# Optimization experiments

Measured on AMD Instinct MI355X. Metric: run time of the kernel, lower is better.

## Reference

```python
import jax, jax.numpy as jnp
import numpy as np

B, S, Z, C, V = 4, 8192, 1024, 1024, 8192
HC, HS, L, NB = 1, 8, 2, 2  # cross heads, self heads, self-attends per block, blocks


def setup_inputs() -> dict:
    key = jax.random.key(0)
    ks = iter(jax.random.split(key, 80))
    nrm = lambda shape, s=0.02: jax.random.normal(next(ks), shape, jnp.float32) * s
    inp = {}
    inp['inputs'] = jax.random.randint(next(ks), (B, S), 0, V)
    inp['emb'] = nrm((V, C))
    inp['c_lnq_g'] = jnp.ones((C,)); inp['c_lnq_b'] = jnp.zeros((C,))
    inp['c_lnkv_g'] = jnp.ones((C,)); inp['c_lnkv_b'] = jnp.zeros((C,))
    for n in ['q', 'k', 'v', 'o']:
        inp[f'c_w{n}'] = nrm((C, C)); inp[f'c_b{n}'] = jnp.zeros((C,))
    inp['c_ln2_g'] = jnp.ones((C,)); inp['c_ln2_b'] = jnp.zeros((C,))
    inp['c_w1'] = nrm((C, C)); inp['c_b1'] = jnp.zeros((C,))
    inp['c_w2'] = nrm((C, C)); inp['c_b2'] = jnp.zeros((C,))
    inp['s_lnq_g'] = jnp.ones((L, C)); inp['s_lnq_b'] = jnp.zeros((L, C))
    for n in ['q', 'k', 'v', 'o']:
        inp[f's_w{n}'] = nrm((L, C, C)); inp[f's_b{n}'] = jnp.zeros((L, C))
    inp['s_ln2_g'] = jnp.ones((L, C)); inp['s_ln2_b'] = jnp.zeros((L, C))
    inp['s_w1'] = nrm((L, C, C)); inp['s_b1'] = jnp.zeros((L, C))
    inp['s_w2'] = nrm((L, C, C)); inp['s_b2'] = jnp.zeros((L, C))
    return inp


def _ln(x, g, b):
    m = x.mean(-1, keepdims=True)
    v = ((x - m) ** 2).mean(-1, keepdims=True)
    return (x - m) * jax.lax.rsqrt(v + 1e-5) * g + b


def _sqrelu(x):
    r = jax.nn.relu(x)
    return r * r


def _attn(qx, kvx, wq, bq, wk, bk, wv, bv, wo, bo, h, mask):
    b, lq, c = qx.shape
    lk = kvx.shape[1]
    d = c // h
    q = (qx @ wq + bq).reshape(b, lq, h, d)
    k = (kvx @ wk + bk).reshape(b, lk, h, d)
    v = (kvx @ wv + bv).reshape(b, lk, h, d)
    s = jnp.einsum('bqhd,bkhd->bhqk', q, k) * (1.0 / np.sqrt(d))
    s = jnp.where(mask, s, jnp.finfo(s.dtype).min)
    a = jax.nn.softmax(s, axis=-1)
    o = jnp.einsum('bhqk,bkhd->bqhd', a, v).reshape(b, lq, c)
    return o @ wo + bo


def _forward(inputs, emb,
             c_lnq_g, c_lnq_b, c_lnkv_g, c_lnkv_b,
             c_wq, c_bq, c_wk, c_bk, c_wv, c_bv, c_wo, c_bo,
             c_ln2_g, c_ln2_b, c_w1, c_b1, c_w2, c_b2,
             s_lnq_g, s_lnq_b, s_wq, s_bq, s_wk, s_bk, s_wv, s_bv, s_wo, s_bo,
             s_ln2_g, s_ln2_b, s_w1, s_b1, s_w2, s_b2):
    e = emb[inputs]                     # [B, S, C] embedded long context
    z = e[:, -Z:, :]                    # latents = last Z embedded positions
    # Perceiver-AR shifted causal cross mask: latent i sits at abs pos (S - Z + i)
    qi = jnp.arange(Z)[:, None]
    ki = jnp.arange(S)[None, :]
    cmask = ki <= (S - Z) + qi          # True = attend allowed, [Z, S]
    zn = _ln(z, c_lnq_g, c_lnq_b)
    en = _ln(e, c_lnkv_g, c_lnkv_b)
    z = z + _attn(zn, en, c_wq, c_bq, c_wk, c_bk, c_wv, c_bv, c_wo, c_bo, HC, cmask)
    h = _ln(z, c_ln2_g, c_ln2_b)
    z = z + _sqrelu(h @ c_w1 + c_b1) @ c_w2 + c_b2
    smask = jnp.tril(jnp.ones((Z, Z), bool))
    for _ in range(NB):                 # weight-shared blocks
        for l in range(L):
            zn = _ln(z, s_lnq_g[l], s_lnq_b[l])
            z = z + _attn(zn, zn, s_wq[l], s_bq[l], s_wk[l], s_bk[l],
                          s_wv[l], s_bv[l], s_wo[l], s_bo[l], HS, smask)
            h = _ln(z, s_ln2_g[l], s_ln2_b[l])
            z = z + _sqrelu(h @ s_w1[l] + s_b1[l]) @ s_w2[l] + s_b2[l]
    return z


def reference(inputs, emb,
              c_lnq_g, c_lnq_b, c_lnkv_g, c_lnkv_b,
              c_wq, c_bq, c_wk, c_bk, c_wv, c_bv, c_wo, c_bo,
              c_ln2_g, c_ln2_b, c_w1, c_b1, c_w2, c_b2,
              s_lnq_g, s_lnq_b, s_wq, s_bq, s_wk, s_bk, s_wv, s_bv, s_wo, s_bo,
              s_ln2_g, s_ln2_b, s_w1, s_b1, s_w2, s_b2):
    return _forward(inputs, emb,
                    c_lnq_g, c_lnq_b, c_lnkv_g, c_lnkv_b,
                    c_wq, c_bq, c_wk, c_bk, c_wv, c_bv, c_wo, c_bo,
                    c_ln2_g, c_ln2_b, c_w1, c_b1, c_w2, c_b2,
                    s_lnq_g, s_lnq_b, s_wq, s_bq, s_wk, s_bk, s_wv, s_bv, s_wo, s_bo,
                    s_ln2_g, s_ln2_b, s_w1, s_b1, s_w2, s_b2)
```

## Files before the change

kernel.cpp:

```cpp
#include <hip/hip_runtime.h>

typedef unsigned short u16;
typedef float f32x4 __attribute__((ext_vector_type(4)));
typedef short s16x8 __attribute__((ext_vector_type(8)));
typedef unsigned short u16x4 __attribute__((ext_vector_type(4)));

__device__ __forceinline__ u16 f2b(float x){
  union{float f; unsigned u;} a; a.f=x;
  return (u16)((a.u + 0x7fffu + ((a.u>>16)&1u))>>16);
}
__device__ __forceinline__ float b2f(u16 x){
  union{unsigned u; float f;} a; a.u = ((unsigned)x)<<16; return a.f;
}

__device__ __forceinline__ void gload16(const u16* g, u16* l){
  __builtin_amdgcn_global_load_lds(
      (const __attribute__((address_space(1))) void*)g,
      (__attribute__((address_space(3))) void*)l, 16, 0, 0);
}

__device__ __forceinline__ float block_reduce(float v, int op, float* sh){
  #pragma unroll
  for (int o=32;o>0;o>>=1){
    float t = __shfl_down(v, o);
    v = op ? fmaxf(v,t) : v+t;
  }
  int w = threadIdx.x>>6;
  if ((threadIdx.x&63)==0) sh[w]=v;
  __syncthreads();
  float r = op ? fmaxf(fmaxf(sh[0],sh[1]),fmaxf(sh[2],sh[3]))
               : (sh[0]+sh[1]+sh[2]+sh[3]);
  __syncthreads();
  return r;
}

template<int EPI, bool BG, int MT>
__global__ __launch_bounds__(256)
void gemm_nt(const u16* __restrict__ A,
             long a_s1, long a_s2, int azd, int lda,
             const u16* __restrict__ B, const int* __restrict__ bidx,
             int bidx_zs, long b_s1, long b_s2, int bzd, int ldb,
             const float* __restrict__ bias, int bias_zs,
             void* __restrict__ Cv, long c_s1, long c_s2, int czd, int ldc,
             int K)
{
  __shared__ u16 lA[MT*32*64];
  __shared__ u16 lB[128*64];
  const int tid = threadIdx.x;
  const int z = blockIdx.z;
  const int m0 = blockIdx.x * (MT*32);
  const int n0 = blockIdx.y * 128;
  const u16* Ab = A + (long)(z/azd)*a_s1 + (long)(z%azd)*a_s2;
  const u16* Bb = B + (long)(z/bzd)*b_s1 + (long)(z%bzd)*b_s2;
  const int* bi = BG ? (bidx + (long)z*bidx_zs) : nullptr;

  const int w = tid >> 6, lane = tid & 63;
  const int wr = w >> 1, wc = w & 1;
  const int lm = lane >> 4, ln = lane & 15;

  f32x4 acc[MT][4];
  #pragma unroll
  for (int i=0;i<MT;i++)
    #pragma unroll
    for (int j=0;j<4;j++) acc[i][j] = (f32x4){0.f,0.f,0.f,0.f};

  for (int kt = 0; kt < K; kt += 64) {
    __syncthreads();
    #pragma unroll
    for (int i = 0; i < MT; i++) {
      int c = i*256 + tid;
      int r = c >> 3;
      int kc = ((c & 7) ^ (r & 7)) << 3;
      gload16(Ab + (long)(m0+r)*lda + kt + kc, &lA[(i*256 + (tid & 192))*8]);
    }
    #pragma unroll
    for (int i = 0; i < 4; i++) {
      int c = i*256 + tid;
      int r = c >> 3;
      int kc = ((c & 7) ^ (r & 7)) << 3;
      long brow = BG ? (long)bi[n0 + r] : (long)(n0 + r);
      gload16(Bb + brow*(long)ldb + kt + kc, &lB[(i*256 + (tid & 192))*8]);
    }
    __syncthreads();
    #pragma unroll
    for (int kk = 0; kk < 2; kk++) {
      const int chunk = kk*4 + lm;
      const int ksw = ((chunk ^ (ln & 7)) << 3);
      s16x8 af[MT], bf[4];
      #pragma unroll
      for (int i=0;i<MT;i++) af[i] = *(const s16x8*)(&lA[(wr*(MT*16) + i*16 + ln)*64 + ksw]);
      #pragma unroll
      for (int j=0;j<4;j++) bf[j] = *(const s16x8*)(&lB[(wc*64 + j*16 + ln)*64 + ksw]);
      #pragma unroll
      for (int i=0;i<MT;i++)
        #pragma unroll
        for (int j=0;j<4;j++)
          acc[i][j] = __builtin_amdgcn_mfma_f32_16x16x32_bf16(bf[j], af[i], acc[i][j], 0,0,0);
    }
  }

  const long co = (long)(z/czd)*c_s1 + (long)(z%czd)*c_s2;
  const float* biasp = (EPI==3 || EPI==5) ? nullptr : (bias + (long)z*bias_zs);
  #pragma unroll
  for (int i=0;i<MT;i++) {
    const int m = m0 + wr*(MT*16) + i*16 + ln;
    #pragma unroll
    for (int j=0;j<4;j++) {
      const int nb = n0 + wc*64 + j*16 + lm*4;
      f32x4 v = acc[i][j];
      if constexpr (EPI == 3) {
        *(f32x4*)((float*)Cv + co + (long)m*ldc + nb) = v;
      } else if constexpr (EPI == 5) {
        u16x4 pk;
        pk[0]=f2b(v[0]*0.03125f); pk[1]=f2b(v[1]*0.03125f);
        pk[2]=f2b(v[2]*0.03125f); pk[3]=f2b(v[3]*0.03125f);
        *(u16x4*)((u16*)Cv + co + (long)m*ldc + nb) = pk;
      } else {
        float4 vb = *(const float4*)(biasp + nb);
        if constexpr (EPI == 2) {
          float* Cf = (float*)Cv + co + (long)m*ldc + nb;
          f32x4 old = *(f32x4*)Cf;
          old[0] += v[0]+vb.x; old[1] += v[1]+vb.y;
          old[2] += v[2]+vb.z; old[3] += v[3]+vb.w;
          *(f32x4*)Cf = old;
        } else {
          float x0 = v[0]+vb.x, x1 = v[1]+vb.y, x2 = v[2]+vb.z, x3 = v[3]+vb.w;
          if constexpr (EPI == 1) {
            x0 = x0>0.f ? x0*x0 : 0.f; x1 = x1>0.f ? x1*x1 : 0.f;
            x2 = x2>0.f ? x2*x2 : 0.f; x3 = x3>0.f ? x3*x3 : 0.f;
          }
          u16x4 pk; pk[0]=f2b(x0); pk[1]=f2b(x1); pk[2]=f2b(x2); pk[3]=f2b(x3);
          *(u16x4*)((u16*)Cv + co + (long)m*ldc + nb) = pk;
        }
      }
    }
  }
}

__global__ __launch_bounds__(256)
void gemm_qkv(const u16* __restrict__ A, const u16* __restrict__ Bw,
              const float* __restrict__ bias,
              u16* __restrict__ Qs, u16* __restrict__ Ks, u16* __restrict__ VsT)
{
  __shared__ u16 lA[64*64];
  __shared__ u16 lB[128*64];
  const int tid = threadIdx.x;
  const int m0 = blockIdx.x * 64;
  const int n0 = blockIdx.y * 128;
  const int w = tid >> 6, lane = tid & 63;
  const int wr = w >> 1, wc = w & 1;
  const int lm = lane >> 4, ln = lane & 15;
  const bool tp = (n0 < 2048);

  f32x4 acc[2][4];
  #pragma unroll
  for (int i=0;i<2;i++)
    #pragma unroll
    for (int j=0;j<4;j++) acc[i][j] = (f32x4){0.f,0.f,0.f,0.f};

  for (int kt = 0; kt < 1024; kt += 64) {
    __syncthreads();
    #pragma unroll
    for (int i = 0; i < 2; i++) {
      int c = i*256 + tid;
      int r = c >> 3;
      int kc = ((c & 7) ^ (r & 7)) << 3;
      gload16(A + (long)(m0+r)*1024 + kt + kc, &lA[(i*256 + (tid & 192))*8]);
    }
    #pragma unroll
    for (int i = 0; i < 4; i++) {
      int c = i*256 + tid;
      int r = c >> 3;
      int kc = ((c & 7) ^ (r & 7)) << 3;
      gload16(Bw + (long)(n0+r)*1024 + kt + kc, &lB[(i*256 + (tid & 192))*8]);
    }
    __syncthreads();
    #pragma unroll
    for (int kk = 0; kk < 2; kk++) {
      const int chunk = kk*4 + lm;
      const int ksw = ((chunk ^ (ln & 7)) << 3);
      s16x8 af[2], bf[4];
      #pragma unroll
      for (int i=0;i<2;i++) af[i] = *(const s16x8*)(&lA[(wr*32 + i*16 + ln)*64 + ksw]);
      #pragma unroll
      for (int j=0;j<4;j++) bf[j] = *(const s16x8*)(&lB[(wc*64 + j*16 + ln)*64 + ksw]);
      if (tp) {
        #pragma unroll
        for (int i=0;i<2;i++)
          #pragma unroll
          for (int j=0;j<4;j++)
            acc[i][j] = __builtin_amdgcn_mfma_f32_16x16x32_bf16(bf[j], af[i], acc[i][j], 0,0,0);
      } else {
        #pragma unroll
        for (int i=0;i<2;i++)
          #pragma unroll
          for (int j=0;j<4;j++)
            acc[i][j] = __builtin_amdgcn_mfma_f32_16x16x32_bf16(af[i], bf[j], acc[i][j], 0,0,0);
      }
    }
  }

  if (tp) {
    u16* dst = (n0 < 1024) ? Qs : Ks;
    #pragma unroll
    for (int i=0;i<2;i++) {
      const int m = m0 + wr*32 + i*16 + ln;
      #pragma unroll
      for (int j=0;j<4;j++) {
        const int gn = n0 + wc*64 + j*16 + lm*4;
        float4 vb = *(const float4*)(bias + gn);
        f32x4 v = acc[i][j];
        u16x4 pk;
        pk[0]=f2b(v[0]+vb.x); pk[1]=f2b(v[1]+vb.y);
        pk[2]=f2b(v[2]+vb.z); pk[3]=f2b(v[3]+vb.w);
        *(u16x4*)(dst + (long)m*1024 + (gn & 1023)) = pk;
      }
    }
  } else {
    #pragma unroll
    for (int i=0;i<2;i++) {
      const int gmb = m0 + wr*32 + i*16 + lm*4;
      #pragma unroll
      for (int j=0;j<4;j++) {
        const int gn = n0 + wc*64 + j*16 + ln;
        const float bb = bias[gn];
        f32x4 v = acc[i][j];
        long addr = (long)(gmb >> 10)*1048576 + (long)(gn - 2048)*1024 + (gmb & 1023);
        u16x4 pk;
        #pragma unroll
        for (int r=0;r<4;r++) pk[r] = f2b(v[r] + bb);
        *(u16x4*)(VsT + addr) = pk;
      }
    }
  }
}

__global__ __launch_bounds__(256)
void flash_self(const u16* __restrict__ Qs, const u16* __restrict__ Ks,
                const u16* __restrict__ VsT, u16* __restrict__ O)
{
  __shared__ u16 lK[64][128];
  __shared__ u16 lV[128][64];
  __shared__ u16 lP[4][16][64];

  const int tid = threadIdx.x;
  const int w = tid >> 6, lane = tid & 63;
  const int g = lane >> 4, ln = lane & 15;
  const int bh = blockIdx.x;
  const int b = bh >> 3, h = bh & 7;
  const int y = blockIdx.y;
  const int qt = (y < 8) ? (15 - y) : (y - 8);

  const long qrow0 = (long)b*1024 + qt*64 + w*16;
  const u16* Qp = Qs + qrow0*1024 + h*128;
  const u16* Kp = Ks + (long)b*1048576 + h*128;
  const u16* Vp = VsT + (long)b*1048576 + (long)h*131072;

  s16x8 bq[4];
  #pragma unroll
  for (int ks=0;ks<4;ks++)
    bq[ks] = *(const s16x8*)(Qp + (long)ln*1024 + ks*32 + g*8);

  f32x4 ao[8];
  #pragma unroll
  for (int i=0;i<8;i++) ao[i] = (f32x4){0.f,0.f,0.f,0.f};
  float mrun = -3.0e38f, lrun = 0.f;
  const int qc = qt*64 + w*16 + ln;

  const int nt = qt + 1;

  s16x8 pK[4], pV[4];
  #pragma unroll
  for (int i=0;i<4;i++){
    int c = i*256 + tid;
    int rr = c >> 4, d8 = c & 15;
    pK[i] = *(const s16x8*)(Kp + (long)rr*1024 + d8*8);
    int dd = c >> 3, k8 = c & 7;
    pV[i] = *(const s16x8*)(Vp + (long)dd*1024 + k8*8);
  }

  for (int kt = 0; kt < nt; ++kt) {
    __syncthreads();
    #pragma unroll
    for (int i=0;i<4;i++){
      int c = i*256 + tid;
      int rr = c >> 4, d8 = c & 15;
      *(s16x8*)(&lK[rr][(d8 ^ (rr&7))*8]) = pK[i];
      int dd = c >> 3, k8 = c & 7;
      *(s16x8*)(&lV[dd][(k8 ^ (dd&7))*8]) = pV[i];
    }
    __syncthreads();
    if (kt+1 < nt){
      const u16* src  = Kp + (long)((kt+1)*64)*1024;
      const u16* vsrc = Vp + (kt+1)*64;
      #pragma unroll
      for (int i=0;i<4;i++){
        int c = i*256 + tid;
        int rr = c >> 4, d8 = c & 15;
        pK[i] = *(const s16x8*)(src + (long)rr*1024 + d8*8);
        int dd = c >> 3, k8 = c & 7;
        pV[i] = *(const s16x8*)(vsrc + (long)dd*1024 + k8*8);
      }
    }

    f32x4 as_[4];
    #pragma unroll
    for (int i=0;i<4;i++) as_[i] = (f32x4){0.f,0.f,0.f,0.f};
    __builtin_amdgcn_s_setprio(1);
    #pragma unroll
    for (int ks=0;ks<4;ks++){
      #pragma unroll
      for (int mi=0;mi<4;mi++){
        s16x8 ak = *(const s16x8*)(&lK[16*mi + ln][((g + 4*ks) ^ (ln&7))*8]);
        as_[mi] = __builtin_amdgcn_mfma_f32_16x16x32_bf16(ak, bq[ks], as_[mi], 0,0,0);
      }
    }
    __builtin_amdgcn_s_setprio(0);

    const int kkb = kt*64 + 4*g;
    float mx = -3.0e38f;
    #pragma unroll
    for (int mi=0;mi<4;mi++)
      #pragma unroll
      for (int r=0;r<4;r++){
        float s = as_[mi][r] * 0.08838834764831845f;
        if (kkb + 16*mi + r > qc) s = -3.0e38f;
        as_[mi][r] = s;
        mx = fmaxf(mx, s);
      }
    mx = fmaxf(mx, __shfl_xor(mx, 16));
    mx = fmaxf(mx, __shfl_xor(mx, 32));
    float mnew = fmaxf(mrun, mx);
    float alpha = __expf(mrun - mnew);
    float sum = 0.f;
    #pragma unroll
    for (int mi=0;mi<4;mi++){
      u16x4 pk;
      #pragma unroll
      for (int r=0;r<4;r++){
        float p = __expf(as_[mi][r] - mnew);
        sum += p;
        pk[r] = f2b(p);
      }
      *(u16x4*)(&lP[w][ln][(((2*mi + (g>>1)) ^ (ln&7))<<3) + (g&1)*4]) = pk;
    }
    sum += __shfl_xor(sum, 16);
    sum += __shfl_xor(sum, 32);
    lrun = lrun*alpha + sum;
    mrun = mnew;
    #pragma unroll
    for (int mi=0;mi<8;mi++)
      #pragma unroll
      for (int r=0;r<4;r++)
        ao[mi][r] *= alpha;

    __builtin_amdgcn_s_setprio(1);
    #pragma unroll
    for (int ks=0;ks<2;ks++){
      s16x8 bp = *(const s16x8*)(&lP[w][ln][((4*ks + g) ^ (ln&7))*8]);
      #pragma unroll
      for (int mi=0;mi<8;mi++){
        s16x8 av = *(const s16x8*)(&lV[16*mi + ln][((g + 4*ks) ^ (ln&7))*8]);
        ao[mi] = __builtin_amdgcn_mfma_f32_16x16x32_bf16(av, bp, ao[mi], 0,0,0);
      }
    }
    __builtin_amdgcn_s_setprio(0);
  }

  const float inv = 1.f/lrun;
  #pragma unroll
  for (int mi=0;mi<8;mi++){
    u16x4 pk;
    #pragma unroll
    for (int r=0;r<4;r++) pk[r] = f2b(ao[mi][r]*inv);
    *(u16x4*)(O + (qrow0 + ln)*1024 + h*128 + 16*mi + 4*g) = pk;
  }
}

__global__ __launch_bounds__(256)
void gather_T(const u16* __restrict__ Vtab, const int* __restrict__ idx,
              u16* __restrict__ VT)
{
  __shared__ u16 t[64][72];
  const int s0 = blockIdx.x*64, d0 = blockIdx.y*64;
  const int tr = threadIdx.x>>3, tc = threadIdx.x&7;
  #pragma unroll
  for (int i=0;i<2;i++){
    int s = tr + i*32;
    long row = idx[s0+s];
    *(s16x8*)(&t[s][tc*8]) = *(const s16x8*)(Vtab + row*1024 + d0 + tc*8);
  }
  __syncthreads();
  #pragma unroll
  for (int i=0;i<2;i++){
    int d = tr + i*32;
    u16 out[8];
    #pragma unroll
    for (int j=0;j<8;j++) out[j] = t[tc*8+j][d];
    *(s16x8*)(VT + (long)(d0+d)*8192 + s0 + tc*8) = *(s16x8*)out;
  }
}

__global__ __launch_bounds__(256)
void reduce8(const float* __restrict__ Pp, u16* __restrict__ Ob){
  long i = ((long)blockIdx.x*256 + threadIdx.x)*4;
  f32x4 s = *(const f32x4*)(Pp + i);
  #pragma unroll
  for (int p=1;p<8;p++){
    f32x4 t = *(const f32x4*)(Pp + (long)p*1048576 + i);
    s[0]+=t[0]; s[1]+=t[1]; s[2]+=t[2]; s[3]+=t[3];
  }
  u16x4 pk;
  #pragma unroll
  for (int r=0;r<4;r++) pk[r] = f2b(s[r]);
  *(u16x4*)(Ob + i) = pk;
}

template<int TWO>
__global__ __launch_bounds__(256)
void ln_kernel(const float* __restrict__ X,
               const float* __restrict__ g1, const float* __restrict__ bb1,
               const float* __restrict__ g2, const float* __restrict__ bb2,
               u16* __restrict__ o1, u16* __restrict__ o2)
{
  __shared__ float sh[4];
  const long row = blockIdx.x;
  const int tid = threadIdx.x;
  const float* x = X + row*1024;
  float4 t = *(const float4*)(x + tid*4);
  float s = t.x+t.y+t.z+t.w;
  float m = block_reduce(s, 0, sh) * (1.f/1024.f);
  float d0=t.x-m, d1=t.y-m, d2=t.z-m, d3=t.w-m;
  float s2 = d0*d0+d1*d1+d2*d2+d3*d3;
  float var = block_reduce(s2, 0, sh) * (1.f/1024.f);
  float r = rsqrtf(var + 1e-5f);
  const int c = tid*4;
  {
    float4 g = *(const float4*)(g1+c);
    float4 b = *(const float4*)(bb1+c);
    u16x4 pk;
    pk[0]=f2b(d0*r*g.x+b.x); pk[1]=f2b(d1*r*g.y+b.y);
    pk[2]=f2b(d2*r*g.z+b.z); pk[3]=f2b(d3*r*g.w+b.w);
    *(u16x4*)(o1 + row*1024 + c) = pk;
  }
  if constexpr (TWO) {
    float4 g = *(const float4*)(g2+c);
    float4 b = *(const float4*)(bb2+c);
    u16x4 pk;
    pk[0]=f2b(d0*r*g.x+b.x); pk[1]=f2b(d1*r*g.y+b.y);
    pk[2]=f2b(d2*r*g.z+b.z); pk[3]=f2b(d3*r*g.w+b.w);
    *(u16x4*)(o2 + row*1024 + c) = pk;
  }
}

template<int LEN>
__global__ __launch_bounds__(256)
void softmax16(u16* __restrict__ S, int qmask, int off)
{
  constexpr int PER = LEN/256;
  __shared__ float sh[4];
  const long row = blockIdx.x;
  const int qi = ((int)row) & qmask;
  const int lim = off + qi;
  u16* srow = S + row*(long)LEN;
  const int tid = threadIdx.x;
  float v[PER];
  float mx = -3.0e38f;
  #pragma unroll
  for (int i=0;i<PER/4;i++){
    int j0 = i*1024 + tid*4;
    u16x4 t = *(const u16x4*)(srow + j0);
    #pragma unroll
    for (int k=0;k<4;k++){
      float val = (j0+k <= lim) ? b2f(t[k]) : -3.0e38f;
      v[i*4+k] = val;
      mx = fmaxf(mx, val);
    }
  }
  float M = block_reduce(mx, 1, sh);
  float s = 0.f;
  #pragma unroll
  for (int i=0;i<PER;i++){ float e = __expf(v[i]-M); v[i]=e; s+=e; }
  float T = block_reduce(s, 0, sh);
  float inv = 1.0f / T;
  #pragma unroll
  for (int i=0;i<PER/4;i++){
    int j0 = i*1024 + tid*4;
    u16x4 pk;
    #pragma unroll
    for (int k=0;k<4;k++) pk[k] = f2b(v[i*4+k]*inv);
    *(u16x4*)(srow + j0) = pk;
  }
}

__global__ __launch_bounds__(256)
void zinit(const int* __restrict__ inputs, const float* __restrict__ emb,
           float* __restrict__ z)
{
  const int row = blockIdx.x;
  const int b = row >> 10, q = row & 1023;
  const int id = inputs[(long)b*8192 + 7168 + q];
  float4 v = *(const float4*)(emb + (long)id*1024 + threadIdx.x*4);
  *(float4*)(z + (long)row*1024 + threadIdx.x*4) = v;
}

__global__ __launch_bounds__(256)
void pack_bias(const float* __restrict__ bq, const float* __restrict__ bk,
               const float* __restrict__ bv, float* __restrict__ qkvb,
               const float* __restrict__ cbk, const float* __restrict__ cbv,
               float* __restrict__ kvb)
{
  const int l = blockIdx.y;
  const int i = blockIdx.x*256 + threadIdx.x;
  float v;
  if (i < 1024)      v = bq[l*1024 + i];
  else if (i < 2048) v = bk[l*1024 + i - 1024];
  else               v = bv[l*1024 + i - 2048];
  qkvb[l*3072 + i] = v;
  if (l == 0 && i < 2048)
    kvb[i] = (i < 1024) ? cbk[i] : cbv[i - 1024];
}

__global__ __launch_bounds__(256)
void transpose_w(const float* cwq, const float* cwk, const float* cwv,
                 const float* cwo, const float* cw1, const float* cw2,
                 const float* swq, const float* swk, const float* swv,
                 const float* swo, const float* sw1, const float* sw2,
                 u16* __restrict__ wT)
{
  const int slot = blockIdx.z;
  const float* W;
  switch (slot) {
    case 0:  W = cwq; break;  case 1:  W = cwk; break;
    case 2:  W = cwv; break;  case 3:  W = cwo; break;
    case 4:  W = cw1; break;  case 5:  W = cw2; break;
    case 6:  W = swq; break;  case 7:  W = swk; break;
    case 8:  W = swv; break;  case 9:  W = swo; break;
    case 10: W = sw1; break;  case 11: W = sw2; break;
    case 12: W = swq + 1048576; break; case 13: W = swk + 1048576; break;
    case 14: W = swv + 1048576; break; case 15: W = swo + 1048576; break;
    case 16: W = sw1 + 1048576; break; default: W = sw2 + 1048576; break;
  }
  u16* T = wT + (long)slot*1048576;
  __shared__ float t[32][33];
  const int tx = threadIdx.x & 31, ty = threadIdx.x >> 5;
  const int k0 = blockIdx.x*32, n0 = blockIdx.y*32;
  #pragma unroll
  for (int i=0;i<4;i++)
    t[ty + i*8][tx] = W[(long)(k0 + ty + i*8)*1024 + n0 + tx];
  __syncthreads();
  #pragma unroll
  for (int i=0;i<4;i++)
    T[(long)(n0 + ty + i*8)*1024 + k0 + tx] = f2b(t[tx][ty + i*8]);
}

extern "C" void kernel_launch(void* const* d_in, const int* in_sizes, int n_in,
                              void* d_out, int out_size, void* d_ws, size_t ws_size,
                              hipStream_t stream)
{
  (void)in_sizes; (void)n_in; (void)out_size;
  const int*   inputs   = (const int*)  d_in[0];
  const float* emb      = (const float*)d_in[1];
  const float* c_lnq_g  = (const float*)d_in[2];
  const float* c_lnq_b  = (const float*)d_in[3];
  const float* c_lnkv_g = (const float*)d_in[4];
  const float* c_lnkv_b = (const float*)d_in[5];
  const float* c_bq = (const float*)d_in[7];
  const float* c_bk = (const float*)d_in[9];
  const float* c_bv = (const float*)d_in[11];
  const float* c_bo = (const float*)d_in[13];
  const float* c_ln2_g = (const float*)d_in[14];
  const float* c_ln2_b = (const float*)d_in[15];
  const float* c_b1 = (const float*)d_in[17];
  const float* c_b2 = (const float*)d_in[19];
  const float* s_lnq_g = (const float*)d_in[20];
  const float* s_lnq_b = (const float*)d_in[21];
  const float* s_bq = (const float*)d_in[23];
  const float* s_bk = (const float*)d_in[25];
  const float* s_bv = (const float*)d_in[27];
  const float* s_bo = (const float*)d_in[29];
  const float* s_ln2_g = (const float*)d_in[30];
  const float* s_ln2_b = (const float*)d_in[31];
  const float* s_b1 = (const float*)d_in[33];
  const float* s_b2 = (const float*)d_in[35];

  const long MB1 = 1048576;
  const long PB  = 8388608;

  char* wsb = (char*)d_ws;
  size_t off = 0;
  auto alloc = [&](size_t n)->char* {
    char* p = wsb + off; off += (n + 255) & ~(size_t)255; return p;
  };
  u16*   wT       = (u16*)  alloc((size_t)18*1048576*2);
  u16*   Ktab     = (u16*)  alloc((size_t)8192*1024*2);
  u16*   Vtab     = (u16*)  alloc((size_t)8192*1024*2);
  u16*   VTcb     = (u16*)  alloc((size_t)1024*8192*2);
  u16*   Q        = (u16*)  alloc((size_t)4096*1024*2);
  u16*   O        = (u16*)  alloc((size_t)4096*1024*2);
  float* Opart    = (float*)alloc((size_t)8*1024*1024*4);
  u16*   P4       = (u16*)  alloc((size_t)4*1024*8192*2);
  u16*   lnkv_tab = P4;
  u16*   zn       = P4 +  8*MB1;
  u16*   h1       = P4 + 12*MB1;
  u16*   Qs       = P4 + 16*MB1;
  u16*   Ks       = P4 + 20*MB1;
  u16*   VsT      = P4 + 24*MB1;
  float* qkvb     = (float*)alloc((size_t)2*3072*4);
  float* kvb      = (float*)alloc((size_t)2048*4);
  float* z        = (float*)d_out;

  if (ws_size < off) return;

  transpose_w<<<dim3(32,32,18), 256, 0, stream>>>(
      (const float*)d_in[6], (const float*)d_in[8], (const float*)d_in[10],
      (const float*)d_in[12], (const float*)d_in[16], (const float*)d_in[18],
      (const float*)d_in[22], (const float*)d_in[24], (const float*)d_in[26],
      (const float*)d_in[28], (const float*)d_in[32], (const float*)d_in[34], wT);
  pack_bias<<<dim3(12,2), 256, 0, stream>>>(s_bq, s_bk, s_bv, qkvb,
                                            c_bk, c_bv, kvb);
  ln_kernel<0><<<8192, 256, 0, stream>>>(emb, c_lnkv_g, c_lnkv_b,
                                         nullptr, nullptr, lnkv_tab, nullptr);
  zinit<<<4096, 256, 0, stream>>>(inputs, emb, z);
  ln_kernel<0><<<4096, 256, 0, stream>>>(z, c_lnq_g, c_lnq_b,
                                         nullptr, nullptr, zn, nullptr);

  gemm_nt<0,false,4><<<dim3(64,8,2),256,0,stream>>>(
      lnkv_tab, 0,0,1, 1024,
      wT + 1*MB1, nullptr, 0, MB1,0,1, 1024,
      kvb, 1024,
      Ktab, PB,0,1, 1024, 1024);
  gemm_nt<0,false,2><<<dim3(64,8,1),256,0,stream>>>(
      zn, 0,0,1, 1024,
      wT + 0*MB1, nullptr, 0, 0,0,1, 1024,
      c_bq, 0,
      Q, 0,0,1, 1024, 1024);
  gemm_nt<5,true,4><<<dim3(8,64,4),256,0,stream>>>(
      Q, MB1,0,1, 1024,
      Ktab, inputs, 8192, 0,0,1, 1024,
      nullptr, 0,
      P4, PB,0,1, 8192, 1024);
  softmax16<8192><<<4096, 256, 0, stream>>>(P4, 1023, 7168);
  for (int b = 0; b < 4; ++b) {
    gather_T<<<dim3(128,16),256,0,stream>>>(Vtab, inputs + (long)b*8192, VTcb);
    gemm_nt<3,false,2><<<dim3(16,8,8),256,0,stream>>>(
        P4 + (long)b*PB, 0,1024,8, 8192,
        VTcb, nullptr, 0, 0,1024,8, 8192,
        nullptr, 0,
        Opart, 1048576,0,1, 1024, 1024);
    reduce8<<<1024,256,0,stream>>>(Opart, O + (long)b*MB1);
  }
  gemm_nt<2,false,2><<<dim3(64,8,1),256,0,stream>>>(
      O, 0,0,1, 1024,
      wT + 3*MB1, nullptr, 0, 0,0,1, 1024,
      c_bo, 0,
      z, 0,0,1, 1024, 1024);

  ln_kernel<0><<<4096,256,0,stream>>>(z, c_ln2_g, c_ln2_b, nullptr,nullptr, zn, nullptr);
  gemm_nt<1,false,2><<<dim3(64,8,1),256,0,stream>>>(
      zn, 0,0,1, 1024,
      wT + 4*MB1, nullptr, 0, 0,0,1, 1024,
      c_b1, 0,
      h1, 0,0,1, 1024, 1024);
  gemm_nt<2,false,2><<<dim3(64,8,1),256,0,stream>>>(
      h1, 0,0,1, 1024,
      wT + 5*MB1, nullptr, 0, 0,0,1, 1024,
      c_b2, 0,
      z, 0,0,1, 1024, 1024);

  for (int it = 0; it < 4; ++it) {
    const int l = it & 1;
    const u16* wqkv = wT + (size_t)(6 + l*6)*MB1;
    const u16* wo = wT + (size_t)(6 + l*6 + 3)*MB1;
    const u16* w1 = wT + (size_t)(6 + l*6 + 4)*MB1;
    const u16* w2 = wT + (size_t)(6 + l*6 + 5)*MB1;

    ln_kernel<0><<<4096,256,0,stream>>>(z, s_lnq_g + l*1024, s_lnq_b + l*1024,
                                        nullptr,nullptr, zn, nullptr);
    gemm_qkv<<<dim3(64,24),256,0,stream>>>(zn, wqkv, qkvb + l*3072, Qs, Ks, VsT);
    flash_self<<<dim3(32,16),256,0,stream>>>(Qs, Ks, VsT, O);
    gemm_nt<2,false,2><<<dim3(64,8,1),256,0,stream>>>(
        O, 0,0,1, 1024,  wo, nullptr, 0, 0,0,1, 1024,
        s_bo + l*1024, 0,
        z, 0,0,1, 1024, 1024);

    ln_kernel<0><<<4096,256,0,stream>>>(z, s_ln2_g + l*1024, s_ln2_b + l*1024,
                                        nullptr,nullptr, zn, nullptr);
    gemm_nt<1,false,2><<<dim3(64,8,1),256,0,stream>>>(
        zn, 0,0,1, 1024,  w1, nullptr, 0, 0,0,1, 1024,
        s_b1 + l*1024, 0,
        h1, 0,0,1, 1024, 1024);
    gemm_nt<2,false,2><<<dim3(64,8,1),256,0,stream>>>(
        h1, 0,0,1, 1024,  w2, nullptr, 0, 0,0,1, 1024,
        s_b2 + l*1024, 0,
        z, 0,0,1, 1024, 1024);
  }
}
```

Baseline: 1.062 ms.

## Swap GEMM grid order, split-K 4-way with bf16 partials, fuse embed+LN

Adds a SWAP template flag so consecutive workgroups walk along N for the same M tile, which changes L2 reuse of A and B tiles in every projection GEMM and in gemm_qkv. The cross-attention PV GEMM moves from 8-way split-K with fp32 partials to 4-way split-K that writes bf16 partials, so the reduce kernel reads a quarter as many bytes at the cost of rounding each partial before the sum. The embedding gather and the first LayerNorm are fused into one kernel, which removes one launch and one full read of z.

```diff
diff --git a/kernel.cpp b/kernel.cpp
--- a/kernel.cpp
+++ b/kernel.cpp
@@ -34,7 +34,7 @@
   return r;
 }
 
-template<int EPI, bool BG, int MT>
+template<int EPI, bool BG, int MT, int SWAP>
 __global__ __launch_bounds__(256)
 void gemm_nt(const u16* __restrict__ A,
              long a_s1, long a_s2, int azd, int lda,
@@ -48,8 +48,8 @@
   __shared__ u16 lB[128*64];
   const int tid = threadIdx.x;
   const int z = blockIdx.z;
-  const int m0 = blockIdx.x * (MT*32);
-  const int n0 = blockIdx.y * 128;
+  const int m0 = (SWAP ? blockIdx.y : blockIdx.x) * (MT*32);
+  const int n0 = (SWAP ? blockIdx.x : blockIdx.y) * 128;
   const u16* Ab = A + (long)(z/azd)*a_s1 + (long)(z%azd)*a_s2;
   const u16* Bb = B + (long)(z/bzd)*b_s1 + (long)(z%bzd)*b_s2;
   const int* bi = BG ? (bidx + (long)z*bidx_zs) : nullptr;
@@ -100,7 +100,7 @@
   }
 
   const long co = (long)(z/czd)*c_s1 + (long)(z%czd)*c_s2;
-  const float* biasp = (EPI==3 || EPI==5) ? nullptr : (bias + (long)z*bias_zs);
+  const float* biasp = (EPI==3 || EPI==5 || EPI==6) ? nullptr : (bias + (long)z*bias_zs);
   #pragma unroll
   for (int i=0;i<MT;i++) {
     const int m = m0 + wr*(MT*16) + i*16 + ln;
@@ -114,6 +114,10 @@
         u16x4 pk;
         pk[0]=f2b(v[0]*0.03125f); pk[1]=f2b(v[1]*0.03125f);
         pk[2]=f2b(v[2]*0.03125f); pk[3]=f2b(v[3]*0.03125f);
+        *(u16x4*)((u16*)Cv + co + (long)m*ldc + nb) = pk;
+      } else if constexpr (EPI == 6) {
+        u16x4 pk;
+        pk[0]=f2b(v[0]); pk[1]=f2b(v[1]); pk[2]=f2b(v[2]); pk[3]=f2b(v[3]);
         *(u16x4*)((u16*)Cv + co + (long)m*ldc + nb) = pk;
       } else {
         float4 vb = *(const float4*)(biasp + nb);
@@ -145,8 +149,8 @@
   __shared__ u16 lA[64*64];
   __shared__ u16 lB[128*64];
   const int tid = threadIdx.x;
-  const int m0 = blockIdx.x * 64;
-  const int n0 = blockIdx.y * 128;
+  const int m0 = blockIdx.y * 64;
+  const int n0 = blockIdx.x * 128;
   const int w = tid >> 6, lane = tid & 63;
   const int wr = w >> 1, wc = w & 1;
   const int lm = lane >> 4, ln = lane & 15;
@@ -402,17 +406,15 @@
 }
 
 __global__ __launch_bounds__(256)
-void reduce8(const float* __restrict__ Pp, u16* __restrict__ Ob){
+void reduce4b(const u16* __restrict__ Pp, u16* __restrict__ Ob){
   long i = ((long)blockIdx.x*256 + threadIdx.x)*4;
-  f32x4 s = *(const f32x4*)(Pp + i);
-  #pragma unroll
-  for (int p=1;p<8;p++){
-    f32x4 t = *(const f32x4*)(Pp + (long)p*1048576 + i);
-    s[0]+=t[0]; s[1]+=t[1]; s[2]+=t[2]; s[3]+=t[3];
-  }
-  u16x4 pk;
-  #pragma unroll
-  for (int r=0;r<4;r++) pk[r] = f2b(s[r]);
+  float s0=0.f, s1=0.f, s2=0.f, s3=0.f;
+  #pragma unroll
+  for (int p=0;p<4;p++){
+    u16x4 t = *(const u16x4*)(Pp + (long)p*1048576 + i);
+    s0 += b2f(t[0]); s1 += b2f(t[1]); s2 += b2f(t[2]); s3 += b2f(t[3]);
+  }
+  u16x4 pk; pk[0]=f2b(s0); pk[1]=f2b(s1); pk[2]=f2b(s2); pk[3]=f2b(s3);
   *(u16x4*)(Ob + i) = pk;
 }
 
@@ -453,6 +455,33 @@
   }
 }
 
+__global__ __launch_bounds__(256)
+void zinit_ln(const int* __restrict__ inputs, const float* __restrict__ emb,
+              const float* __restrict__ g1, const float* __restrict__ bb1,
+              float* __restrict__ z, u16* __restrict__ zn)
+{
+  __shared__ float sh[4];
+  const int row = blockIdx.x;
+  const int b = row >> 10, q = row & 1023;
+  const int id = inputs[(long)b*8192 + 7168 + q];
+  const int tid = threadIdx.x;
+  float4 t = *(const float4*)(emb + (long)id*1024 + tid*4);
+  *(float4*)(z + (long)row*1024 + tid*4) = t;
+  float s = t.x+t.y+t.z+t.w;
+  float m = block_reduce(s, 0, sh) * (1.f/1024.f);
+  float d0=t.x-m, d1=t.y-m, d2=t.z-m, d3=t.w-m;
+  float s2 = d0*d0+d1*d1+d2*d2+d3*d3;
+  float var = block_reduce(s2, 0, sh) * (1.f/1024.f);
+  float r = rsqrtf(var + 1e-5f);
+  const int c = tid*4;
+  float4 g = *(const float4*)(g1+c);
+  float4 bb = *(const float4*)(bb1+c);
+  u16x4 pk;
+  pk[0]=f2b(d0*r*g.x+bb.x); pk[1]=f2b(d1*r*g.y+bb.y);
+  pk[2]=f2b(d2*r*g.z+bb.z); pk[3]=f2b(d3*r*g.w+bb.w);
+  *(u16x4*)(zn + (long)row*1024 + c) = pk;
+}
+
 template<int LEN>
 __global__ __launch_bounds__(256)
 void softmax16(u16* __restrict__ S, int qmask, int off)
@@ -491,17 +520,6 @@
     for (int k=0;k<4;k++) pk[k] = f2b(v[i*4+k]*inv);
     *(u16x4*)(srow + j0) = pk;
   }
-}
-
-__global__ __launch_bounds__(256)
-void zinit(const int* __restrict__ inputs, const float* __restrict__ emb,
-           float* __restrict__ z)
-{
-  const int row = blockIdx.x;
-  const int b = row >> 10, q = row & 1023;
-  const int id = inputs[(long)b*8192 + 7168 + q];
-  float4 v = *(const float4*)(emb + (long)id*1024 + threadIdx.x*4);
-  *(float4*)(z + (long)row*1024 + threadIdx.x*4) = v;
 }
 
 __global__ __launch_bounds__(256)
@@ -598,7 +616,7 @@
   u16*   VTcb     = (u16*)  alloc((size_t)1024*8192*2);
   u16*   Q        = (u16*)  alloc((size_t)4096*1024*2);
   u16*   O        = (u16*)  alloc((size_t)4096*1024*2);
-  float* Opart    = (float*)alloc((size_t)8*1024*1024*4);
+  u16*   Opart16  = (u16*)  alloc((size_t)8*1024*1024*4);
   u16*   P4       = (u16*)  alloc((size_t)4*1024*8192*2);
   u16*   lnkv_tab = P4;
   u16*   zn       = P4 +  8*MB1;
@@ -621,21 +639,19 @@
                                             c_bk, c_bv, kvb);
   ln_kernel<0><<<8192, 256, 0, stream>>>(emb, c_lnkv_g, c_lnkv_b,
                                          nullptr, nullptr, lnkv_tab, nullptr);
-  zinit<<<4096, 256, 0, stream>>>(inputs, emb, z);
-  ln_kernel<0><<<4096, 256, 0, stream>>>(z, c_lnq_g, c_lnq_b,
-                                         nullptr, nullptr, zn, nullptr);
-
-  gemm_nt<0,false,4><<<dim3(64,8,2),256,0,stream>>>(
+  zinit_ln<<<4096, 256, 0, stream>>>(inputs, emb, c_lnq_g, c_lnq_b, z, zn);
+
+  gemm_nt<0,false,4,1><<<dim3(8,64,2),256,0,stream>>>(
       lnkv_tab, 0,0,1, 1024,
       wT + 1*MB1, nullptr, 0, MB1,0,1, 1024,
       kvb, 1024,
       Ktab, PB,0,1, 1024, 1024);
-  gemm_nt<0,false,2><<<dim3(64,8,1),256,0,stream>>>(
+  gemm_nt<0,false,2,1><<<dim3(8,64,1),256,0,stream>>>(
       zn, 0,0,1, 1024,
       wT + 0*MB1, nullptr, 0, 0,0,1, 1024,
       c_bq, 0,
       Q, 0,0,1, 1024, 1024);
-  gemm_nt<5,true,4><<<dim3(8,64,4),256,0,stream>>>(
+  gemm_nt<5,true,4,1><<<dim3(64,8,4),256,0,stream>>>(
       Q, MB1,0,1, 1024,
       Ktab, inputs, 8192, 0,0,1, 1024,
       nullptr, 0,
@@ -643,26 +659,26 @@
   softmax16<8192><<<4096, 256, 0, stream>>>(P4, 1023, 7168);
   for (int b = 0; b < 4; ++b) {
     gather_T<<<dim3(128,16),256,0,stream>>>(Vtab, inputs + (long)b*8192, VTcb);
-    gemm_nt<3,false,2><<<dim3(16,8,8),256,0,stream>>>(
-        P4 + (long)b*PB, 0,1024,8, 8192,
-        VTcb, nullptr, 0, 0,1024,8, 8192,
+    gemm_nt<6,false,2,1><<<dim3(8,16,4),256,0,stream>>>(
+        P4 + (long)b*PB, 0,2048,4, 8192,
+        VTcb, nullptr, 0, 0,2048,4, 8192,
         nullptr, 0,
-        Opart, 1048576,0,1, 1024, 1024);
-    reduce8<<<1024,256,0,stream>>>(Opart, O + (long)b*MB1);
-  }
-  gemm_nt<2,false,2><<<dim3(64,8,1),256,0,stream>>>(
+        Opart16, 1048576,0,1, 1024, 2048);
+    reduce4b<<<1024,256,0,stream>>>(Opart16, O + (long)b*MB1);
+  }
+  gemm_nt<2,false,2,1><<<dim3(8,64,1),256,0,stream>>>(
       O, 0,0,1, 1024,
       wT + 3*MB1, nullptr, 0, 0,0,1, 1024,
       c_bo, 0,
       z, 0,0,1, 1024, 1024);
 
   ln_kernel<0><<<4096,256,0,stream>>>(z, c_ln2_g, c_ln2_b, nullptr,nullptr, zn, nullptr);
-  gemm_nt<1,false,2><<<dim3(64,8,1),256,0,stream>>>(
+  gemm_nt<1,false,2,1><<<dim3(8,64,1),256,0,stream>>>(
       zn, 0,0,1, 1024,
       wT + 4*MB1, nullptr, 0, 0,0,1, 1024,
       c_b1, 0,
       h1, 0,0,1, 1024, 1024);
-  gemm_nt<2,false,2><<<dim3(64,8,1),256,0,stream>>>(
+  gemm_nt<2,false,2,1><<<dim3(8,64,1),256,0,stream>>>(
       h1, 0,0,1, 1024,
       wT + 5*MB1, nullptr, 0, 0,0,1, 1024,
       c_b2, 0,
@@ -677,20 +693,20 @@
 
     ln_kernel<0><<<4096,256,0,stream>>>(z, s_lnq_g + l*1024, s_lnq_b + l*1024,
                                         nullptr,nullptr, zn, nullptr);
-    gemm_qkv<<<dim3(64,24),256,0,stream>>>(zn, wqkv, qkvb + l*3072, Qs, Ks, VsT);
+    gemm_qkv<<<dim3(24,64),256,0,stream>>>(zn, wqkv, qkvb + l*3072, Qs, Ks, VsT);
     flash_self<<<dim3(32,16),256,0,stream>>>(Qs, Ks, VsT, O);
-    gemm_nt<2,false,2><<<dim3(64,8,1),256,0,stream>>>(
+    gemm_nt<2,false,2,1><<<dim3(8,64,1),256,0,stream>>>(
         O, 0,0,1, 1024,  wo, nullptr, 0, 0,0,1, 1024,
         s_bo + l*1024, 0,
         z, 0,0,1, 1024, 1024);
 
     ln_kernel<0><<<4096,256,0,stream>>>(z, s_ln2_g + l*1024, s_ln2_b + l*1024,
                                         nullptr,nullptr, zn, nullptr);
-    gemm_nt<1,false,2><<<dim3(64,8,1),256,0,stream>>>(
+    gemm_nt<1,false,2,1><<<dim3(8,64,1),256,0,stream>>>(
         zn, 0,0,1, 1024,  w1, nullptr, 0, 0,0,1, 1024,
         s_b1 + l*1024, 0,
         h1, 0,0,1, 1024, 1024);
-    gemm_nt<2,false,2><<<dim3(64,8,1),256,0,stream>>>(
+    gemm_nt<2,false,2,1><<<dim3(8,64,1),256,0,stream>>>(
         h1, 0,0,1, 1024,  w2, nullptr, 0, 0,0,1, 1024,
         s_b2 + l*1024, 0,
         z, 0,0,1, 1024, 1024);
```

Result: no change. 1.075 ms (+1.2%).
